# Optimization experiments

Hardware: AMD Instinct MI355X
Metric: run time of the kernel (lower is better)

Reference implementation:

```python
import jax, jax.numpy as jnp
import numpy as np

B, L, S, H, E, D = 4, 2048, 2048, 8, 64, 64

def setup_inputs() -> dict:
    key = jax.random.key(0)
    kq, kk, kv = jax.random.split(key, 3)
    queries = jax.random.normal(kq, (B, L, H, E), dtype=jnp.float32)
    keys = jax.random.normal(kk, (B, S, H, E), dtype=jnp.float32)
    values = jax.random.normal(kv, (B, S, H, D), dtype=jnp.float32)
    return {"queries": queries, "keys": keys, "values": values}

def reference(queries, keys, values):
    # scale = self.scale or 1/sqrt(E)
    scale = 1.0 / jnp.sqrt(jnp.float32(queries.shape[-1]))
    # scores: [B, H, L, S]
    scores = jnp.einsum('blhe,bshe->bhls', queries, keys)
    # dropout is identity at inference (Keras Dropout only active in training)
    A = jax.nn.softmax(scale * scores, axis=-1)
    # output: [B, L, H, D]
    return jnp.einsum('bhls,bshd->blhd', A, values)
```

## Files before the change

### kernel.cpp

```cpp
#include <hip/hip_runtime.h>


#define B_ 4
#define L_ 2048
#define S_ 2048
#define H_ 8
#define E_ 64
#define D_ 64

typedef __attribute__((ext_vector_type(8))) __bf16 bf16x8;
typedef __attribute__((ext_vector_type(2))) __bf16 bf16x2;
typedef __attribute__((ext_vector_type(4))) float floatx4;

#define KSTR 72
#define VSTR 40
#define PSTR 40

__device__ __forceinline__ bf16x8 cvt8(float4 a, float4 b) {
  bf16x8 r;
  r[0] = (__bf16)a.x; r[1] = (__bf16)a.y; r[2] = (__bf16)a.z; r[3] = (__bf16)a.w;
  r[4] = (__bf16)b.x; r[5] = (__bf16)b.y; r[6] = (__bf16)b.z; r[7] = (__bf16)b.w;
  return r;
}

__global__ __launch_bounds__(256) void attn_kernel(const float* __restrict__ Q,
                                                   const float* __restrict__ K,
                                                   const float* __restrict__ V,
                                                   float* __restrict__ O) {
  __shared__ __align__(16) __bf16 K_lds[2][32 * KSTR];
  __shared__ __align__(16) __bf16 Vt_lds[2][64 * VSTR];
  __shared__ __align__(16) __bf16 P_lds[4 * 16 * PSTR];

  const int tid = threadIdx.x;
  const int lane = tid & 63;
  const int wave = tid >> 6;
  const int n16 = lane & 15;
  const int quad = lane >> 4;

  const int bid = blockIdx.x;
  const int qb = bid & 31;
  const int h = (bid >> 5) & 7;
  const int b = bid >> 8;

  const float qscale = 0.125f * 1.44269504088896340736f;
  const int qrow = qb * 64 + wave * 16 + n16;
  const float* qp = Q + ((size_t)(b * L_ + qrow) * H_ + h) * E_;
  bf16x8 qf0, qf1;
  {
    float4 a0 = *(const float4*)(qp + quad * 8);
    float4 a1 = *(const float4*)(qp + quad * 8 + 4);
    float4 b0 = *(const float4*)(qp + 32 + quad * 8);
    float4 b1 = *(const float4*)(qp + 32 + quad * 8 + 4);
    bf16x8 q0 = cvt8(a0, a1), q1 = cvt8(b0, b1);
#pragma unroll
    for (int j = 0; j < 8; ++j) {
      qf0[j] = (__bf16)((float)q0[j] * qscale);
      qf1[j] = (__bf16)((float)q1[j] * qscale);
    }
  }

  float l[4];
  floatx4 o[4];
#pragma unroll
  for (int r = 0; r < 4; ++r) l[r] = 0.0f;
#pragma unroll
  for (int dc = 0; dc < 4; ++dc) o[dc] = (floatx4){0.f, 0.f, 0.f, 0.f};

  const int kr = tid >> 3;
  const int kc = (tid & 7) * 8;
  const float* kbase = K + ((size_t)b * S_ * H_ + h) * E_;
  const int vu = tid & 15;
  const int vdb = (tid >> 4) * 4;
  const float* vbase = V + ((size_t)b * S_ * H_ + h) * D_;

  __bf16* Pw = &P_lds[wave * 16 * PSTR];

  {
    const float* gk = kbase + (size_t)kr * H_ * E_ + kc;
    float4 ka = *(const float4*)gk;
    float4 kb = *(const float4*)(gk + 4);
    *(bf16x8*)&K_lds[0][kr * KSTR + kc] = cvt8(ka, kb);
    const float* gv = vbase + (size_t)vu * H_ * D_ + vdb;
    float4 va = *(const float4*)gv;
    float4 vb = *(const float4*)(gv + 16 * H_ * D_);
    float lo[4] = {va.x, va.y, va.z, va.w};
    float hi[4] = {vb.x, vb.y, vb.z, vb.w};
#pragma unroll
    for (int j = 0; j < 4; ++j) {
      bf16x2 pp = {(__bf16)lo[j], (__bf16)hi[j]};
      *(bf16x2*)&Vt_lds[0][(vdb + j) * VSTR + 2 * vu] = pp;
    }
  }

  const int NT = S_ / 32;
  for (int t = 0; t < NT; ++t) {
    const int buf = t & 1;
    __syncthreads();

    float4 ka, kb, va, vb;
    const bool stage = (t + 1 < NT);
    if (stage) {
      const int ks2 = (t + 1) * 32;
      const float* gk = kbase + (size_t)(ks2 + kr) * H_ * E_ + kc;
      ka = *(const float4*)gk;
      kb = *(const float4*)(gk + 4);
      const float* gv = vbase + (size_t)(ks2 + vu) * H_ * D_ + vdb;
      va = *(const float4*)gv;
      vb = *(const float4*)(gv + 16 * H_ * D_);
    }

    floatx4 sc0 = (floatx4){0.f, 0.f, 0.f, 0.f};
    floatx4 sc1 = (floatx4){0.f, 0.f, 0.f, 0.f};
    {
      const __bf16* Kb = K_lds[buf];
      bf16x8 k00 = *(const bf16x8*)&Kb[n16 * KSTR + quad * 8];
      bf16x8 k01 = *(const bf16x8*)&Kb[n16 * KSTR + 32 + quad * 8];
      bf16x8 k10 = *(const bf16x8*)&Kb[(16 + n16) * KSTR + quad * 8];
      bf16x8 k11 = *(const bf16x8*)&Kb[(16 + n16) * KSTR + 32 + quad * 8];
      sc0 = __builtin_amdgcn_mfma_f32_16x16x32_bf16(qf0, k00, sc0, 0, 0, 0);
      sc0 = __builtin_amdgcn_mfma_f32_16x16x32_bf16(qf1, k01, sc0, 0, 0, 0);
      sc1 = __builtin_amdgcn_mfma_f32_16x16x32_bf16(qf0, k10, sc1, 0, 0, 0);
      sc1 = __builtin_amdgcn_mfma_f32_16x16x32_bf16(qf1, k11, sc1, 0, 0, 0);
    }

#pragma unroll
    for (int r = 0; r < 4; ++r) {
      float p0 = __builtin_amdgcn_exp2f(sc0[r]);
      float p1 = __builtin_amdgcn_exp2f(sc1[r]);
      l[r] += p0 + p1;
      bf16x2 pp = {(__bf16)p0, (__bf16)p1};
      *(bf16x2*)&Pw[(quad * 4 + r) * PSTR + 2 * n16] = pp;
    }

    if (stage) {
      *(bf16x8*)&K_lds[buf ^ 1][kr * KSTR + kc] = cvt8(ka, kb);
      float lo[4] = {va.x, va.y, va.z, va.w};
      float hi[4] = {vb.x, vb.y, vb.z, vb.w};
#pragma unroll
      for (int j = 0; j < 4; ++j) {
        bf16x2 pp = {(__bf16)lo[j], (__bf16)hi[j]};
        *(bf16x2*)&Vt_lds[buf ^ 1][(vdb + j) * VSTR + 2 * vu] = pp;
      }
    }

    __syncthreads();

    {
      bf16x8 pf = *(const bf16x8*)&Pw[n16 * PSTR + quad * 8];
      const __bf16* Vb = Vt_lds[buf];
#pragma unroll
      for (int dc = 0; dc < 4; ++dc) {
        bf16x8 vfr = *(const bf16x8*)&Vb[(dc * 16 + n16) * VSTR + quad * 8];
        o[dc] = __builtin_amdgcn_mfma_f32_16x16x32_bf16(pf, vfr, o[dc], 0, 0, 0);
      }
    }
  }

  float* ob = O + ((size_t)(b * L_ + qb * 64 + wave * 16) * H_ + h) * D_;
#pragma unroll
  for (int r = 0; r < 4; ++r) {
    float lr = l[r];
    lr += __shfl_xor(lr, 1);
    lr += __shfl_xor(lr, 2);
    lr += __shfl_xor(lr, 4);
    lr += __shfl_xor(lr, 8);
    float inv = 1.0f / lr;
    float* orow = ob + (size_t)(quad * 4 + r) * H_ * D_;
#pragma unroll
    for (int dc = 0; dc < 4; ++dc) orow[dc * 16 + n16] = o[dc][r] * inv;
  }
}

extern "C" void kernel_launch(void* const* d_in, const int* in_sizes, int n_in,
                              void* d_out, int out_size, void* d_ws, size_t ws_size,
                              hipStream_t stream) {
  const float* Q = (const float*)d_in[0];
  const float* K = (const float*)d_in[1];
  const float* V = (const float*)d_in[2];
  float* O = (float*)d_out;
  dim3 grid(B_ * H_ * (L_ / 64));
  attn_kernel<<<grid, 256, 0, stream>>>(Q, K, V, O);
}
```

Measured before the change: 160.3 us.

## Switch attention to 32x32x16 MFMA with 128-row query tiles per block

Replaces the 16x16x32 bf16 MFMA tiling with 32x32x16 MFMA, computing transposed scores (K as the A operand) so that each wave owns 32 query rows, and each block covers 128 queries instead of 64. Each K/V tile staged into LDS is therefore reused across twice as many queries, halving global K/V traffic and conversion work per query. Row sums no longer need a multi-step shuffle reduction, and outputs are written as float4. In exchange the grid shrinks to 512 blocks, which lowers occupancy and parallelism, and the LDS strides and V staging layout change, which may cause bank conflicts.

```diff
diff --git a/kernel.cpp b/kernel.cpp
--- a/kernel.cpp
+++ b/kernel.cpp
@@ -9,12 +9,13 @@
 #define D_ 64
 
 typedef __attribute__((ext_vector_type(8))) __bf16 bf16x8;
+typedef __attribute__((ext_vector_type(4))) __bf16 bf16x4;
 typedef __attribute__((ext_vector_type(2))) __bf16 bf16x2;
-typedef __attribute__((ext_vector_type(4))) float floatx4;
+typedef __attribute__((ext_vector_type(16))) float floatx16;
 
 #define KSTR 72
-#define VSTR 40
-#define PSTR 40
+#define VSTR 36
+#define PSTR 36
 
 __device__ __forceinline__ bf16x8 cvt8(float4 a, float4 b) {
   bf16x8 r;
@@ -29,42 +30,37 @@
                                                    float* __restrict__ O) {
   __shared__ __align__(16) __bf16 K_lds[2][32 * KSTR];
   __shared__ __align__(16) __bf16 Vt_lds[2][64 * VSTR];
-  __shared__ __align__(16) __bf16 P_lds[4 * 16 * PSTR];
+  __shared__ __align__(16) __bf16 P_lds[4][32 * PSTR];
 
   const int tid = threadIdx.x;
   const int lane = tid & 63;
   const int wave = tid >> 6;
-  const int n16 = lane & 15;
-  const int quad = lane >> 4;
+  const int q32 = lane & 31;
+  const int h32 = lane >> 5;
 
   const int bid = blockIdx.x;
-  const int qb = bid & 31;
-  const int h = (bid >> 5) & 7;
-  const int b = bid >> 8;
+  const int qb = bid & 15;
+  const int h = (bid >> 4) & 7;
+  const int b = bid >> 7;
 
   const float qscale = 0.125f * 1.44269504088896340736f;
-  const int qrow = qb * 64 + wave * 16 + n16;
+  const int qrow = qb * 128 + wave * 32 + q32;
   const float* qp = Q + ((size_t)(b * L_ + qrow) * H_ + h) * E_;
-  bf16x8 qf0, qf1;
-  {
-    float4 a0 = *(const float4*)(qp + quad * 8);
-    float4 a1 = *(const float4*)(qp + quad * 8 + 4);
-    float4 b0 = *(const float4*)(qp + 32 + quad * 8);
-    float4 b1 = *(const float4*)(qp + 32 + quad * 8 + 4);
-    bf16x8 q0 = cvt8(a0, a1), q1 = cvt8(b0, b1);
+  bf16x8 qf[4];
 #pragma unroll
-    for (int j = 0; j < 8; ++j) {
-      qf0[j] = (__bf16)((float)q0[j] * qscale);
-      qf1[j] = (__bf16)((float)q1[j] * qscale);
-    }
+  for (int c = 0; c < 4; ++c) {
+    const float* p = qp + c * 16 + h32 * 8;
+    float4 a = *(const float4*)p;
+    float4 bb = *(const float4*)(p + 4);
+    float t[8] = {a.x, a.y, a.z, a.w, bb.x, bb.y, bb.z, bb.w};
+#pragma unroll
+    for (int j = 0; j < 8; ++j) qf[c][j] = (__bf16)(t[j] * qscale);
   }
 
-  float l[4];
-  floatx4 o[4];
+  float l = 0.0f;
+  floatx16 ot[2];
 #pragma unroll
-  for (int r = 0; r < 4; ++r) l[r] = 0.0f;
-#pragma unroll
-  for (int dc = 0; dc < 4; ++dc) o[dc] = (floatx4){0.f, 0.f, 0.f, 0.f};
+  for (int r = 0; r < 16; ++r) { ot[0][r] = 0.f; ot[1][r] = 0.f; }
 
   const int kr = tid >> 3;
   const int kc = (tid & 7) * 8;
@@ -73,16 +69,16 @@
   const int vdb = (tid >> 4) * 4;
   const float* vbase = V + ((size_t)b * S_ * H_ + h) * D_;
 
-  __bf16* Pw = &P_lds[wave * 16 * PSTR];
+  __bf16* Pw = P_lds[wave];
 
   {
     const float* gk = kbase + (size_t)kr * H_ * E_ + kc;
     float4 ka = *(const float4*)gk;
     float4 kb = *(const float4*)(gk + 4);
     *(bf16x8*)&K_lds[0][kr * KSTR + kc] = cvt8(ka, kb);
-    const float* gv = vbase + (size_t)vu * H_ * D_ + vdb;
+    const float* gv = vbase + (size_t)(2 * vu) * H_ * D_ + vdb;
     float4 va = *(const float4*)gv;
-    float4 vb = *(const float4*)(gv + 16 * H_ * D_);
+    float4 vb = *(const float4*)(gv + H_ * D_);
     float lo[4] = {va.x, va.y, va.z, va.w};
     float hi[4] = {vb.x, vb.y, vb.z, vb.w};
 #pragma unroll
@@ -104,32 +100,32 @@
       const float* gk = kbase + (size_t)(ks2 + kr) * H_ * E_ + kc;
       ka = *(const float4*)gk;
       kb = *(const float4*)(gk + 4);
-      const float* gv = vbase + (size_t)(ks2 + vu) * H_ * D_ + vdb;
+      const float* gv = vbase + (size_t)(ks2 + 2 * vu) * H_ * D_ + vdb;
       va = *(const float4*)gv;
-      vb = *(const float4*)(gv + 16 * H_ * D_);
+      vb = *(const float4*)(gv + H_ * D_);
     }
 
-    floatx4 sc0 = (floatx4){0.f, 0.f, 0.f, 0.f};
-    floatx4 sc1 = (floatx4){0.f, 0.f, 0.f, 0.f};
+    floatx16 sc;
+#pragma unroll
+    for (int r = 0; r < 16; ++r) sc[r] = 0.f;
     {
       const __bf16* Kb = K_lds[buf];
-      bf16x8 k00 = *(const bf16x8*)&Kb[n16 * KSTR + quad * 8];
-      bf16x8 k01 = *(const bf16x8*)&Kb[n16 * KSTR + 32 + quad * 8];
-      bf16x8 k10 = *(const bf16x8*)&Kb[(16 + n16) * KSTR + quad * 8];
-      bf16x8 k11 = *(const bf16x8*)&Kb[(16 + n16) * KSTR + 32 + quad * 8];
-      sc0 = __builtin_amdgcn_mfma_f32_16x16x32_bf16(qf0, k00, sc0, 0, 0, 0);
-      sc0 = __builtin_amdgcn_mfma_f32_16x16x32_bf16(qf1, k01, sc0, 0, 0, 0);
-      sc1 = __builtin_amdgcn_mfma_f32_16x16x32_bf16(qf0, k10, sc1, 0, 0, 0);
-      sc1 = __builtin_amdgcn_mfma_f32_16x16x32_bf16(qf1, k11, sc1, 0, 0, 0);
+#pragma unroll
+      for (int c = 0; c < 4; ++c) {
+        bf16x8 kA = *(const bf16x8*)&Kb[q32 * KSTR + c * 16 + h32 * 8];
+        sc = __builtin_amdgcn_mfma_f32_32x32x16_bf16(kA, qf[c], sc, 0, 0, 0);
+      }
     }
 
 #pragma unroll
-    for (int r = 0; r < 4; ++r) {
-      float p0 = __builtin_amdgcn_exp2f(sc0[r]);
-      float p1 = __builtin_amdgcn_exp2f(sc1[r]);
-      l[r] += p0 + p1;
-      bf16x2 pp = {(__bf16)p0, (__bf16)p1};
-      *(bf16x2*)&Pw[(quad * 4 + r) * PSTR + 2 * n16] = pp;
+    for (int g = 0; g < 4; ++g) {
+      float p0 = __builtin_amdgcn_exp2f(sc[4 * g + 0]);
+      float p1 = __builtin_amdgcn_exp2f(sc[4 * g + 1]);
+      float p2 = __builtin_amdgcn_exp2f(sc[4 * g + 2]);
+      float p3 = __builtin_amdgcn_exp2f(sc[4 * g + 3]);
+      l += (p0 + p1) + (p2 + p3);
+      bf16x4 pp = {(__bf16)p0, (__bf16)p1, (__bf16)p2, (__bf16)p3};
+      *(bf16x4*)&Pw[q32 * PSTR + g * 8 + h32 * 4] = pp;
     }
 
     if (stage) {
@@ -146,28 +142,30 @@
     __syncthreads();
 
     {
-      bf16x8 pf = *(const bf16x8*)&Pw[n16 * PSTR + quad * 8];
       const __bf16* Vb = Vt_lds[buf];
 #pragma unroll
-      for (int dc = 0; dc < 4; ++dc) {
-        bf16x8 vfr = *(const bf16x8*)&Vb[(dc * 16 + n16) * VSTR + quad * 8];
-        o[dc] = __builtin_amdgcn_mfma_f32_16x16x32_bf16(pf, vfr, o[dc], 0, 0, 0);
+      for (int s2 = 0; s2 < 2; ++s2) {
+        bf16x8 pB = *(const bf16x8*)&Pw[q32 * PSTR + s2 * 16 + h32 * 8];
+#pragma unroll
+        for (int dt = 0; dt < 2; ++dt) {
+          bf16x8 vA = *(const bf16x8*)&Vb[(dt * 32 + q32) * VSTR + s2 * 16 + h32 * 8];
+          ot[dt] = __builtin_amdgcn_mfma_f32_32x32x16_bf16(vA, pB, ot[dt], 0, 0, 0);
+        }
       }
     }
   }
 
-  float* ob = O + ((size_t)(b * L_ + qb * 64 + wave * 16) * H_ + h) * D_;
+  l += __shfl_xor(l, 32);
+  const float inv = 1.0f / l;
+  float* orow = O + ((size_t)(b * L_ + qrow) * H_ + h) * D_;
 #pragma unroll
-  for (int r = 0; r < 4; ++r) {
-    float lr = l[r];
-    lr += __shfl_xor(lr, 1);
-    lr += __shfl_xor(lr, 2);
-    lr += __shfl_xor(lr, 4);
-    lr += __shfl_xor(lr, 8);
-    float inv = 1.0f / lr;
-    float* orow = ob + (size_t)(quad * 4 + r) * H_ * D_;
+  for (int dt = 0; dt < 2; ++dt) {
 #pragma unroll
-    for (int dc = 0; dc < 4; ++dc) orow[dc * 16 + n16] = o[dc][r] * inv;
+    for (int g = 0; g < 4; ++g) {
+      float4 v = {ot[dt][4 * g + 0] * inv, ot[dt][4 * g + 1] * inv,
+                  ot[dt][4 * g + 2] * inv, ot[dt][4 * g + 3] * inv};
+      *(float4*)(orow + dt * 32 + g * 8 + h32 * 4) = v;
+    }
   }
 }
 
@@ -178,6 +176,6 @@
   const float* K = (const float*)d_in[1];
   const float* V = (const float*)d_in[2];
   float* O = (float*)d_out;
-  dim3 grid(B_ * H_ * (L_ / 64));
+  dim3 grid(B_ * H_ * (L_ / 128));
   attn_kernel<<<grid, 256, 0, stream>>>(Q, K, V, O);
 }
```

Measured after the change: 198.9 us. 1.24x slower.
